# Kernel tuning notes

Measured on AMD Instinct MI355X. Metric: run time of the kernel, lower is better.

Reference implementation:

```python
import jax, jax.numpy as jnp
import numpy as np

N_NODES = 50000


def _sage_conv(x, src, dst, Wl, Wr, b):
    # PyG SAGEConv (aggr='mean'): out = lin_l(mean_{j in N(i)} x_j) + lin_r(x_i)
    msgs = x[src]                                              # [E, d] gather
    s = jax.ops.segment_sum(msgs, dst, num_segments=N_NODES)   # [N, d]
    cnt = jax.ops.segment_sum(jnp.ones((src.shape[0], 1), x.dtype), dst,
                              num_segments=N_NODES)            # [N, 1]
    agg = s / jnp.maximum(cnt, 1.0)                            # mean, 0 if no nbrs
    return agg @ Wl.T + x @ Wr.T + b


def setup_inputs() -> dict:
    key = jax.random.key(0)
    ks = jax.random.split(key, 12)
    in_dim, h = 128, 128
    E, P = 500000, 200000
    x = jax.random.normal(ks[0], (N_NODES, in_dim), dtype=jnp.float32)
    edge_index = jax.random.randint(ks[1], (2, E), 0, N_NODES)
    pairs = jax.random.randint(ks[2], (P, 2), 0, N_NODES)
    def lin(k, fan_out, fan_in):
        bound = 1.0 / np.sqrt(fan_in)
        return jax.random.uniform(k, (fan_out, fan_in), jnp.float32, -bound, bound)
    return {
        "x": x, "edge_index": edge_index, "pairs": pairs,
        "Wl1": lin(ks[3], h, in_dim), "Wr1": lin(ks[4], h, in_dim),
        "b1": jnp.zeros((h,), jnp.float32),
        "Wl2": lin(ks[5], h, h), "Wr2": lin(ks[6], h, h),
        "b2": jnp.zeros((h,), jnp.float32),
        "W3": lin(ks[7], h, 2 * h), "b3": jnp.zeros((h,), jnp.float32),
        "W4": lin(ks[8], 1, h), "b4": jnp.zeros((1,), jnp.float32),
    }


def reference(x, edge_index, pairs, Wl1, Wr1, b1, Wl2, Wr2, b2, W3, b3, W4, b4):
    src, dst = edge_index[0], edge_index[1]
    h1 = jax.nn.relu(_sage_conv(x, src, dst, Wl1, Wr1, b1))    # [N, h]
    h2 = jax.nn.relu(_sage_conv(h1, src, dst, Wl2, Wr2, b2))   # [N, h]
    a = h2[pairs[:, 0]]                                        # [P, h]
    b = h2[pairs[:, 1]]                                        # [P, h]
    z = jnp.concatenate([a, b], axis=1)                        # [P, 2h]
    s = jax.nn.relu(z @ W3.T + b3) @ W4.T + b4                 # [P, 1]
    return jax.nn.sigmoid(s).squeeze(-1)                       # [P]
```

## Files before the change

kernel.cpp:

```cpp
#include <hip/hip_runtime.h>
#include <math.h>

#define N_NODES 50000
#define E_EDGES 500000
#define P_PAIRS 200000
#define MAX_DEG 64

typedef __bf16    bf16x8 __attribute__((ext_vector_type(8)));
typedef _Float16  f16x8  __attribute__((ext_vector_type(8)));
typedef float     f32x4  __attribute__((ext_vector_type(4)));


#define CONV_BLKS 6250
#define FILL_BLKS 1954
#define PREP_BLKS 128

__global__ __launch_bounds__(256) void fused_pre_k(
        const float* __restrict__ x, __bf16* __restrict__ xb,
        const int* __restrict__ src, const int* __restrict__ dst,
        int* __restrict__ fil, unsigned short* __restrict__ slots,
        const float* __restrict__ Wl1, const float* __restrict__ Wr1,
        const float* __restrict__ Wl2, const float* __restrict__ Wr2,
        const float* __restrict__ W3,
        __bf16* __restrict__ P1, __bf16* __restrict__ P2, __bf16* __restrict__ P4) {
    int b = blockIdx.x, t = threadIdx.x;
    if (b < CONV_BLKS) {
        int i = b * 256 + t;
        float4 v = ((const float4*)x)[i];
        __bf16* o = xb + (size_t)i * 4;
        o[0] = (__bf16)v.x; o[1] = (__bf16)v.y; o[2] = (__bf16)v.z; o[3] = (__bf16)v.w;
    } else if (b < CONV_BLKS + FILL_BLKS) {
        int e = (b - CONV_BLKS) * 256 + t;
        if (e < E_EDGES) {
            int d = dst[e];
            int pos = atomicAdd(&fil[d], 1);
            if (pos < MAX_DEG)
                slots[d * MAX_DEG + pos] = (unsigned short)src[e];
        }
    } else {
        int i = (b - CONV_BLKS - FILL_BLKS) * 256 + t;
        int lane = (i >> 3) & 63;
        int j = i & 7;
        int kq = (lane >> 4) * 8 + j;
        {
            int kt = i >> 12, nt = (i >> 9) & 7;
            int n = nt * 16 + (lane & 15);
            int k = kt * 32 + kq;
            P1[i] = (__bf16)((k < 128) ? Wl1[n * 128 + k] : Wr1[n * 128 + (k - 128)]);
            P2[i] = (__bf16)((k < 128) ? Wl2[n * 128 + k] : Wr2[n * 128 + (k - 128)]);
        }
        {
            int kt = i >> 13, nt = (i >> 9) & 15;
            int n = nt * 16 + (lane & 15);
            int k = kt * 32 + kq;
            P4[i] = (__bf16)((n < 128) ? W3[n * 256 + k] : W3[(n - 128) * 256 + 128 + k]);
        }
    }
}


__global__ __launch_bounds__(256) void agg1_k(const __bf16* __restrict__ feat,
                                              const int* __restrict__ fil,
                                              const unsigned short* __restrict__ slots,
                                              __bf16* __restrict__ agg) {
    int n = blockIdx.x * 4 + (threadIdx.x >> 6);
    if (n >= N_NODES) return;
    int lane = threadIdx.x & 63;
    int slot = lane >> 4, l = lane & 15;
    int deg = fil[n];
    int nit = (deg < MAX_DEG) ? deg : MAX_DEG;

    int ed = (lane < nit) ? (int)slots[n * MAX_DEG + lane] : 0;

    float s[8];
    #pragma unroll
    for (int e = 0; e < 8; ++e) s[e] = 0.f;

    int trips = (nit + 3) >> 2;
    int it = slot;
    int k = 0;
    for (; k + 1 < trips; k += 2, it += 8) {
        int sn0 = __builtin_amdgcn_ds_bpermute(it << 2, ed);
        int sn1 = __builtin_amdgcn_ds_bpermute((it + 4) << 2, ed);
        bf16x8 v0 = *(const bf16x8*)(feat + (size_t)sn0 * 128 + l * 8);
        bf16x8 v1 = *(const bf16x8*)(feat + (size_t)sn1 * 128 + l * 8);
        if (it < nit) {
            #pragma unroll
            for (int e = 0; e < 8; ++e) s[e] += (float)v0[e];
        }
        if (it + 4 < nit) {
            #pragma unroll
            for (int e = 0; e < 8; ++e) s[e] += (float)v1[e];
        }
    }
    if (k < trips) {
        int sn = __builtin_amdgcn_ds_bpermute(it << 2, ed);
        bf16x8 v = *(const bf16x8*)(feat + (size_t)sn * 128 + l * 8);
        if (it < nit) {
            #pragma unroll
            for (int e = 0; e < 8; ++e) s[e] += (float)v[e];
        }
    }

    #pragma unroll
    for (int e = 0; e < 8; ++e) {
        s[e] += __shfl_xor(s[e], 16, 64);
        s[e] += __shfl_xor(s[e], 32, 64);
    }

    if (slot == 0) {
        float inv = 1.0f / fmaxf((float)deg, 1.0f);
        bf16x8 o;
        #pragma unroll
        for (int e = 0; e < 8; ++e) o[e] = (__bf16)(s[e] * inv);
        *(bf16x8*)(agg + (size_t)n * 128 + l * 8) = o;
    }
}


__global__ __launch_bounds__(256) void layer_mfma_k(const __bf16* __restrict__ agg,
                                                    const __bf16* __restrict__ feat,
                                                    const __bf16* __restrict__ wpack,
                                                    const float* __restrict__ bias,
                                                    __bf16* __restrict__ out) {
    int wave = threadIdx.x >> 6;
    int lane = threadIdx.x & 63;
    int m = lane & 15, quad = lane >> 4;
    int rbase = blockIdx.x * 64 + wave * 16;
    int r0 = rbase + m; if (r0 > N_NODES - 1) r0 = N_NODES - 1;

    f32x4 acc[8];
    #pragma unroll
    for (int nt = 0; nt < 8; ++nt) acc[nt] = (f32x4)0.f;

    #pragma unroll
    for (int kt = 0; kt < 8; ++kt) {
        const __bf16* src = (kt < 4) ? agg : feat;
        int ko = (kt & 3) * 32 + quad * 8;
        bf16x8 a0 = *(const bf16x8*)(src + (size_t)r0 * 128 + ko);
        const __bf16* wb = wpack + (size_t)kt * 4096 + lane * 8;
        #pragma unroll
        for (int nt = 0; nt < 8; ++nt) {
            bf16x8 b = *(const bf16x8*)(wb + nt * 512);
            acc[nt] = __builtin_amdgcn_mfma_f32_16x16x32_bf16(a0, b, acc[nt], 0, 0, 0);
        }
    }

    #pragma unroll
    for (int r = 0; r < 4; ++r) {
        int row = rbase + quad * 4 + r;
        if (row < N_NODES) {
            #pragma unroll
            for (int nt = 0; nt < 8; ++nt) {
                float v = acc[nt][r] + bias[nt * 16 + m];
                out[(size_t)row * 128 + nt * 16 + m] = (__bf16)fmaxf(v, 0.f);
            }
        }
    }
}


__global__ __launch_bounds__(256) void layer2uv_k(const __bf16* __restrict__ agg,
                                                  const __bf16* __restrict__ feat,
                                                  const __bf16* __restrict__ wpack,
                                                  const float* __restrict__ bias,
                                                  const __bf16* __restrict__ wpack4,
                                                  _Float16* __restrict__ UV) {
    __shared__ __bf16 sh[4][16][136];
    int wave = threadIdx.x >> 6;
    int lane = threadIdx.x & 63;
    int m = lane & 15, q = lane >> 4;
    int rbase = blockIdx.x * 64 + wave * 16;
    int r0 = rbase + m; if (r0 > N_NODES - 1) r0 = N_NODES - 1;

    f32x4 acc[8];
    #pragma unroll
    for (int nt = 0; nt < 8; ++nt) acc[nt] = (f32x4)0.f;

    #pragma unroll
    for (int kt = 0; kt < 8; ++kt) {
        const __bf16* src = (kt < 4) ? agg : feat;
        int ko = (kt & 3) * 32 + q * 8;
        bf16x8 a0 = *(const bf16x8*)(src + (size_t)r0 * 128 + ko);
        const __bf16* wb = wpack + (size_t)kt * 4096 + lane * 8;
        #pragma unroll
        for (int nt = 0; nt < 8; ++nt) {
            bf16x8 b = *(const bf16x8*)(wb + nt * 512);
            acc[nt] = __builtin_amdgcn_mfma_f32_16x16x32_bf16(a0, b, acc[nt], 0, 0, 0);
        }
    }

    #pragma unroll
    for (int rr = 0; rr < 4; ++rr)
        #pragma unroll
        for (int nt = 0; nt < 8; ++nt) {
            float v = acc[nt][rr] + bias[nt * 16 + m];
            sh[wave][q * 4 + rr][nt * 16 + m] = (__bf16)fmaxf(v, 0.f);
        }

    f32x4 acc2[16];
    #pragma unroll
    for (int nt = 0; nt < 16; ++nt) acc2[nt] = (f32x4)0.f;

    #pragma unroll
    for (int kt = 0; kt < 4; ++kt) {
        bf16x8 a = *(const bf16x8*)&sh[wave][m][kt * 32 + q * 8];
        const __bf16* wb = wpack4 + (size_t)kt * 8192 + lane * 8;
        #pragma unroll
        for (int nt = 0; nt < 16; ++nt) {
            bf16x8 b = *(const bf16x8*)(wb + nt * 512);
            acc2[nt] = __builtin_amdgcn_mfma_f32_16x16x32_bf16(a, b, acc2[nt], 0, 0, 0);
        }
    }

    #pragma unroll
    for (int rr = 0; rr < 4; ++rr) {
        int row = rbase + q * 4 + rr;
        if (row < N_NODES) {
            #pragma unroll
            for (int nt = 0; nt < 16; ++nt)
                UV[(size_t)row * 256 + nt * 16 + m] = (_Float16)acc2[nt][rr];
        }
    }
}


__global__ __launch_bounds__(256) void pair_ep_k(const _Float16* __restrict__ UV,
                                                 const int* __restrict__ pairs,
                                                 const float* __restrict__ b3,
                                                 const float* __restrict__ W4,
                                                 const float* __restrict__ b4,
                                                 float* __restrict__ out) {
    int t = threadIdx.x;
    int g = t >> 4, l = t & 15;
    int base = blockIdx.x * 64;

    float4 b3a = *(const float4*)(b3 + l * 8);
    float4 b3b = *(const float4*)(b3 + l * 8 + 4);
    float4 w4a = *(const float4*)(W4 + l * 8);
    float4 w4b = *(const float4*)(W4 + l * 8 + 4);
    float bb[8] = {b3a.x, b3a.y, b3a.z, b3a.w, b3b.x, b3b.y, b3b.z, b3b.w};
    float ww[8] = {w4a.x, w4a.y, w4a.z, w4a.w, w4b.x, w4b.y, w4b.z, w4b.w};
    float b4s = b4[0];

    int2 pr[4];
    #pragma unroll
    for (int i = 0; i < 4; ++i) pr[i] = ((const int2*)pairs)[base + i * 16 + g];

    f16x8 ua[4], vb[4];
    #pragma unroll
    for (int i = 0; i < 4; ++i) {
        ua[i] = *(const f16x8*)(UV + (size_t)pr[i].x * 256 + l * 8);
        vb[i] = *(const f16x8*)(UV + (size_t)pr[i].y * 256 + 128 + l * 8);
    }

    #pragma unroll
    for (int i = 0; i < 4; ++i) {
        float p = 0.f;
        #pragma unroll
        for (int e = 0; e < 8; ++e)
            p += fmaxf((float)ua[i][e] + (float)vb[i][e] + bb[e], 0.f) * ww[e];
        #pragma unroll
        for (int s = 1; s < 16; s <<= 1) p += __shfl_xor(p, s, 64);
        if (l == 0)
            out[base + i * 16 + g] = 1.0f / (1.0f + expf(-(p + b4s)));
    }
}


extern "C" void kernel_launch(void* const* d_in, const int* in_sizes, int n_in,
                              void* d_out, int out_size, void* d_ws, size_t ws_size,
                              hipStream_t stream) {
    const float* x   = (const float*)d_in[0];
    const int*   ei  = (const int*)d_in[1];
    const int*   prs = (const int*)d_in[2];
    const float* Wl1 = (const float*)d_in[3];
    const float* Wr1 = (const float*)d_in[4];
    const float* b1  = (const float*)d_in[5];
    const float* Wl2 = (const float*)d_in[6];
    const float* Wr2 = (const float*)d_in[7];
    const float* b2  = (const float*)d_in[8];
    const float* W3  = (const float*)d_in[9];
    const float* b3  = (const float*)d_in[10];
    const float* W4  = (const float*)d_in[11];
    const float* b4  = (const float*)d_in[12];
    float* out = (float*)d_out;

    const int* srcv = ei;
    const int* dstv = ei + E_EDGES;

    char* ws = (char*)d_ws;
    size_t off = 0;
    auto alloc = [&](size_t bytes) -> void* {
        void* p = ws + off;
        off = (off + bytes + 255) & ~(size_t)255;
        return p;
    };
    int*            fil    = (int*)alloc(sizeof(int) * N_NODES);
    unsigned short* slots  = (unsigned short*)alloc(sizeof(unsigned short) * (size_t)N_NODES * MAX_DEG);
    __bf16*   P1     = (__bf16*)alloc(sizeof(__bf16) * 32768);
    __bf16*   P2     = (__bf16*)alloc(sizeof(__bf16) * 32768);
    __bf16*   P4     = (__bf16*)alloc(sizeof(__bf16) * 32768);
    __bf16*   xb     = (__bf16*)alloc(sizeof(__bf16) * (size_t)N_NODES * 128);
    __bf16*   aggb   = (__bf16*)alloc(sizeof(__bf16) * (size_t)N_NODES * 128);
    __bf16*   h1b    = (__bf16*)alloc(sizeof(__bf16) * (size_t)N_NODES * 128);
    _Float16* UV     = (_Float16*)alloc(sizeof(_Float16) * (size_t)N_NODES * 256);
    (void)ws_size; (void)in_sizes; (void)n_in; (void)out_size;

    hipMemsetAsync(fil, 0, sizeof(int) * N_NODES, stream);

    fused_pre_k<<<CONV_BLKS + FILL_BLKS + PREP_BLKS, 256, 0, stream>>>(
        x, xb, srcv, dstv, fil, slots, Wl1, Wr1, Wl2, Wr2, W3, P1, P2, P4);

    agg1_k<<<(N_NODES + 3) / 4, 256, 0, stream>>>(xb, fil, slots, aggb);
    layer_mfma_k<<<(N_NODES + 63) / 64, 256, 0, stream>>>(aggb, xb, P1, b1, h1b);
    agg1_k<<<(N_NODES + 3) / 4, 256, 0, stream>>>(h1b, fil, slots, aggb);
    layer2uv_k<<<(N_NODES + 63) / 64, 256, 0, stream>>>(aggb, h1b, P2, b2, P4, UV);
    pair_ep_k<<<P_PAIRS / 64, 256, 0, stream>>>(UV, prs, b3, W4, b4, out);
}
```

Baseline: 225.6 us.

## Build neighbor slot table via bucketed counting sort instead of global atomics

Replaces the per-edge global atomicAdd fill of the per-node slot table with a two-level counting sort. Edges are first bucketed by destination in groups of 256 nodes using shared-memory histograms, a scan and a block-local placement. Each bucket's slot rows are then assembled in shared memory and written out with coalesced stores. This removes contended global atomics and scattered 2-byte writes, at the cost of three extra kernel launches and an extra pass over the edge data through an intermediate buffer.

After: 221.9 us. Within noise of the previous version (-1.7%).

```diff
diff --git a/kernel.cpp b/kernel.cpp
--- a/kernel.cpp
+++ b/kernel.cpp
@@ -6,39 +6,47 @@
 #define P_PAIRS 200000
 #define MAX_DEG 64
 
+#define NB        196
+#define EB        4096
+#define EPT       16
+#define SORT_BLKS 123
+
 typedef __bf16    bf16x8 __attribute__((ext_vector_type(8)));
 typedef _Float16  f16x8  __attribute__((ext_vector_type(8)));
 typedef float     f32x4  __attribute__((ext_vector_type(4)));
 
 
 #define CONV_BLKS 6250
-#define FILL_BLKS 1954
 #define PREP_BLKS 128
 
-__global__ __launch_bounds__(256) void fused_pre_k(
+__global__ __launch_bounds__(256) void pre_k(
         const float* __restrict__ x, __bf16* __restrict__ xb,
-        const int* __restrict__ src, const int* __restrict__ dst,
-        int* __restrict__ fil, unsigned short* __restrict__ slots,
+        const int* __restrict__ dst,
+        int* __restrict__ bucketCnt, int* __restrict__ blockBase,
         const float* __restrict__ Wl1, const float* __restrict__ Wr1,
         const float* __restrict__ Wl2, const float* __restrict__ Wr2,
         const float* __restrict__ W3,
         __bf16* __restrict__ P1, __bf16* __restrict__ P2, __bf16* __restrict__ P4) {
+    __shared__ int cnt[NB];
     int b = blockIdx.x, t = threadIdx.x;
-    if (b < CONV_BLKS) {
-        int i = b * 256 + t;
+    if (b < SORT_BLKS) {
+        if (t < NB) cnt[t] = 0;
+        __syncthreads();
+        int ebase = b * EB;
+        #pragma unroll
+        for (int i = 0; i < EPT; ++i) {
+            int e = ebase + i * 256 + t;
+            if (e < E_EDGES) atomicAdd(&cnt[dst[e] >> 8], 1);
+        }
+        __syncthreads();
+        if (t < NB) blockBase[b * NB + t] = atomicAdd(&bucketCnt[t], cnt[t]);
+    } else if (b < SORT_BLKS + CONV_BLKS) {
+        int i = (b - SORT_BLKS) * 256 + t;
         float4 v = ((const float4*)x)[i];
         __bf16* o = xb + (size_t)i * 4;
         o[0] = (__bf16)v.x; o[1] = (__bf16)v.y; o[2] = (__bf16)v.z; o[3] = (__bf16)v.w;
-    } else if (b < CONV_BLKS + FILL_BLKS) {
-        int e = (b - CONV_BLKS) * 256 + t;
-        if (e < E_EDGES) {
-            int d = dst[e];
-            int pos = atomicAdd(&fil[d], 1);
-            if (pos < MAX_DEG)
-                slots[d * MAX_DEG + pos] = (unsigned short)src[e];
-        }
     } else {
-        int i = (b - CONV_BLKS - FILL_BLKS) * 256 + t;
+        int i = (b - SORT_BLKS - CONV_BLKS) * 256 + t;
         int lane = (i >> 3) & 63;
         int j = i & 7;
         int kq = (lane >> 4) * 8 + j;
@@ -59,15 +67,127 @@
 }
 
 
+__global__ __launch_bounds__(256) void scan_k(const int* __restrict__ bucketCnt,
+                                              int* __restrict__ bucketBase) {
+    __shared__ int buf[256];
+    int t = threadIdx.x;
+    int v = (t < NB) ? bucketCnt[t] : 0;
+    buf[t] = v;
+    __syncthreads();
+    for (int off = 1; off < 256; off <<= 1) {
+        int xv = (t >= off) ? buf[t - off] : 0;
+        __syncthreads();
+        buf[t] += xv;
+        __syncthreads();
+    }
+    if (t < NB) bucketBase[t] = buf[t] - v;
+}
+
+
+__global__ __launch_bounds__(256) void place_k(const int* __restrict__ src,
+                                               const int* __restrict__ dst,
+                                               const int* __restrict__ bucketBase,
+                                               const int* __restrict__ blockBase,
+                                               unsigned* __restrict__ edgebuf) {
+    __shared__ int cnt[256];
+    __shared__ int buf[256];
+    __shared__ int sbase[NB];
+    __shared__ int gbase[NB];
+    __shared__ int cur[NB];
+    __shared__ unsigned sortbuf[EB];
+    __shared__ unsigned char bktof[EB];
+    int blk = blockIdx.x, t = threadIdx.x;
+    cnt[t] = 0;
+    if (t < NB) cur[t] = 0;
+    __syncthreads();
+
+    unsigned packed[EPT];
+    int bk[EPT];
+    int ebase = blk * EB;
+    #pragma unroll
+    for (int i = 0; i < EPT; ++i) {
+        int e = ebase + i * 256 + t;
+        if (e < E_EDGES) {
+            int d = dst[e];
+            packed[i] = ((unsigned)d << 16) | (unsigned)src[e];
+            bk[i] = d >> 8;
+            atomicAdd(&cnt[bk[i]], 1);
+        } else bk[i] = -1;
+    }
+    __syncthreads();
+
+    int v = cnt[t];
+    buf[t] = v;
+    __syncthreads();
+    for (int off = 1; off < 256; off <<= 1) {
+        int xv = (t >= off) ? buf[t - off] : 0;
+        __syncthreads();
+        buf[t] += xv;
+        __syncthreads();
+    }
+    if (t < NB) {
+        sbase[t] = buf[t] - v;
+        gbase[t] = bucketBase[t] + blockBase[blk * NB + t];
+    }
+    __syncthreads();
+
+    #pragma unroll
+    for (int i = 0; i < EPT; ++i) {
+        if (bk[i] >= 0) {
+            int p = sbase[bk[i]] + atomicAdd(&cur[bk[i]], 1);
+            sortbuf[p] = packed[i];
+            bktof[p] = (unsigned char)bk[i];
+        }
+    }
+    __syncthreads();
+
+    int nE = E_EDGES - ebase; if (nE > EB) nE = EB;
+    for (int i = t; i < nE; i += 256) {
+        int bb = bktof[i];
+        edgebuf[gbase[bb] + (i - sbase[bb])] = sortbuf[i];
+    }
+}
+
+
+__global__ __launch_bounds__(256) void slots_k(const unsigned* __restrict__ edgebuf,
+                                               const int* __restrict__ bucketCnt,
+                                               const int* __restrict__ bucketBase,
+                                               unsigned short* __restrict__ slots,
+                                               int* __restrict__ deg) {
+    __shared__ unsigned short srow[256 * MAX_DEG];
+    __shared__ int cur[256];
+    int b = blockIdx.x, t = threadIdx.x;
+    cur[t] = 0;
+    __syncthreads();
+    int base = bucketBase[b], n = bucketCnt[b];
+    for (int i = t; i < n; i += 256) {
+        unsigned p = edgebuf[base + i];
+        int dl = (p >> 16) & 255;
+        int pos = atomicAdd(&cur[dl], 1);
+        if (pos < MAX_DEG) srow[dl * MAX_DEG + pos] = (unsigned short)(p & 0xFFFFu);
+    }
+    __syncthreads();
+    unsigned* sl32 = (unsigned*)slots;
+    const unsigned* sr32 = (const unsigned*)srow;
+    int gbase32 = b * 8192;
+    for (int i = t; i < 8192; i += 256) {
+        int node = b * 256 + (i >> 5);
+        if (node < N_NODES) sl32[gbase32 + i] = sr32[i];
+    }
+    int node = b * 256 + t;
+    if (node < N_NODES) deg[node] = cur[t];
+}
+
+
 __global__ __launch_bounds__(256) void agg1_k(const __bf16* __restrict__ feat,
-                                              const int* __restrict__ fil,
+                                              const int* __restrict__ deg_a,
                                               const unsigned short* __restrict__ slots,
                                               __bf16* __restrict__ agg) {
     int n = blockIdx.x * 4 + (threadIdx.x >> 6);
     if (n >= N_NODES) return;
     int lane = threadIdx.x & 63;
     int slot = lane >> 4, l = lane & 15;
-    int deg = fil[n];
+    int deg = deg_a[n];
     int nit = (deg < MAX_DEG) ? deg : MAX_DEG;
 
     int ed = (lane < nit) ? (int)slots[n * MAX_DEG + lane] : 0;
@@ -296,8 +416,12 @@
         off = (off + bytes + 255) & ~(size_t)255;
         return p;
     };
-    int*            fil    = (int*)alloc(sizeof(int) * N_NODES);
-    unsigned short* slots  = (unsigned short*)alloc(sizeof(unsigned short) * (size_t)N_NODES * MAX_DEG);
+    int*            bucketCnt  = (int*)alloc(sizeof(int) * NB);
+    int*            bucketBase = (int*)alloc(sizeof(int) * NB);
+    int*            blockBase  = (int*)alloc(sizeof(int) * SORT_BLKS * NB);
+    unsigned*       edgebuf    = (unsigned*)alloc(sizeof(unsigned) * E_EDGES);
+    int*            deg        = (int*)alloc(sizeof(int) * N_NODES);
+    unsigned short* slots      = (unsigned short*)alloc(sizeof(unsigned short) * (size_t)N_NODES * MAX_DEG + 512);
     __bf16*   P1     = (__bf16*)alloc(sizeof(__bf16) * 32768);
     __bf16*   P2     = (__bf16*)alloc(sizeof(__bf16) * 32768);
     __bf16*   P4     = (__bf16*)alloc(sizeof(__bf16) * 32768);
@@ -307,14 +431,17 @@
     _Float16* UV     = (_Float16*)alloc(sizeof(_Float16) * (size_t)N_NODES * 256);
     (void)ws_size; (void)in_sizes; (void)n_in; (void)out_size;
 
-    hipMemsetAsync(fil, 0, sizeof(int) * N_NODES, stream);
-
-    fused_pre_k<<<CONV_BLKS + FILL_BLKS + PREP_BLKS, 256, 0, stream>>>(
-        x, xb, srcv, dstv, fil, slots, Wl1, Wr1, Wl2, Wr2, W3, P1, P2, P4);
-
-    agg1_k<<<(N_NODES + 3) / 4, 256, 0, stream>>>(xb, fil, slots, aggb);
+    hipMemsetAsync(bucketCnt, 0, sizeof(int) * NB, stream);
+
+    pre_k<<<SORT_BLKS + CONV_BLKS + PREP_BLKS, 256, 0, stream>>>(
+        x, xb, dstv, bucketCnt, blockBase, Wl1, Wr1, Wl2, Wr2, W3, P1, P2, P4);
+    scan_k<<<1, 256, 0, stream>>>(bucketCnt, bucketBase);
+    place_k<<<SORT_BLKS, 256, 0, stream>>>(srcv, dstv, bucketBase, blockBase, edgebuf);
+    slots_k<<<NB, 256, 0, stream>>>(edgebuf, bucketCnt, bucketBase, slots, deg);
+
+    agg1_k<<<(N_NODES + 3) / 4, 256, 0, stream>>>(xb, deg, slots, aggb);
     layer_mfma_k<<<(N_NODES + 63) / 64, 256, 0, stream>>>(aggb, xb, P1, b1, h1b);
-    agg1_k<<<(N_NODES + 3) / 4, 256, 0, stream>>>(h1b, fil, slots, aggb);
+    agg1_k<<<(N_NODES + 3) / 4, 256, 0, stream>>>(h1b, deg, slots, aggb);
     layer2uv_k<<<(N_NODES + 63) / 64, 256, 0, stream>>>(aggb, h1b, P2, b2, P4, UV);
     pair_ep_k<<<P_PAIRS / 64, 256, 0, stream>>>(UV, prs, b3, W4, b4, out);
 }
```
